# Performance work log

Hardware: AMD Instinct MI355X
Metric: run time of the kernel (lower is better)

## Reference

```python
import jax, jax.numpy as jnp
import numpy as np

B, N, L, K = 2, 16384, 256, 4
DIN, DOUT, DLAT, H, A, NH = 2, 3, 64, 128, 32, 4
PI = float(np.pi)

def _lin(key, din, dout, std=None):
    k1, k2 = jax.random.split(key)
    if std is None:
        lim = 1.0 / np.sqrt(din)
        w = jax.random.uniform(k1, (din, dout), minval=-lim, maxval=lim)
        b = jax.random.uniform(k2, (dout,), minval=-lim, maxval=lim)
        return w, b
    return jax.random.normal(k1, (din, dout)) * std

def setup_inputs() -> dict:
    key = jax.random.key(0)
    ks = jax.random.split(key, 16)
    x = jax.random.uniform(ks[0], (B, N, DIN)) * 2.0 - 1.0
    p = jax.random.uniform(ks[1], (B, L, DIN)) * 2.0 - 1.0
    c = jax.random.normal(ks[2], (B, L, DLAT))
    g = jax.random.uniform(ks[3], (B, L, 1)) * 0.5 + 0.1
    W_stem, b_stem = _lin(ks[4], DLAT, H)
    Wq_sin = _lin(ks[5], DIN, H // 2, std=2.0)
    Wq1, bq1 = _lin(ks[6], H + DIN, H)
    Wq2, bq2 = _lin(ks[7], H, NH * A)
    Wv_sin = _lin(ks[8], DIN, H // 2, std=20.0)
    Wv1, bv1 = _lin(ks[9], H + DIN, H)
    Wv2, bv2 = _lin(ks[10], H, 2 * H)
    Wk, bk = _lin(ks[11], H, NH * A)
    Wv, bv = _lin(ks[12], H, NH * H)
    Wo1, bo1 = _lin(ks[13], NH * H, NH * H)
    Wo2, bo2 = _lin(ks[14], NH * H, DOUT)
    return dict(x=x, p=p, c=c, g=g, W_stem=W_stem, b_stem=b_stem,
                Wq_sin=Wq_sin, Wq1=Wq1, bq1=bq1, Wq2=Wq2, bq2=bq2,
                Wv_sin=Wv_sin, Wv1=Wv1, bv1=bv1, Wv2=Wv2, bv2=bv2,
                Wk=Wk, bk=bk, Wv=Wv, bv=bv, Wo1=Wo1, bo1=bo1, Wo2=Wo2, bo2=bo2)

def _sin_emb(coords, W):
    c = PI * (coords + 1.0)
    e = c @ W
    return jnp.sin(jnp.concatenate([c, e, e + PI / 2.0], axis=-1))

def _emb_mlp(coords, Wsin, W1, b1, W2, b2):
    h = _sin_emb(coords, Wsin)
    h = jax.nn.gelu(h @ W1 + b1, approximate=False)
    return h @ W2 + b2

def _gather(t, idx):
    # t: [B,L,D], idx: [B,N,K] -> [B,N,K,D]
    return jax.vmap(lambda tb, ib: tb[ib])(t, idx)

def reference(x, p, c, g, W_stem, b_stem, Wq_sin, Wq1, bq1, Wq2, bq2,
              Wv_sin, Wv1, bv1, Wv2, bv2, Wk, bk, Wv, bv, Wo1, bo1, Wo2, bo2):
    c = c @ W_stem + b_stem                       # [B,L,H]
    k = c @ Wk + bk                               # [B,L,NH*A]
    rel_pos = x[:, :, None, :] - p[:, None, :, :] # [B,N,L,2]
    zx = jnp.sum(rel_pos ** 2, axis=-1)           # [B,N,L]
    idx = jnp.argsort(zx, axis=-1)[:, :, :K]      # [B,N,K]
    zx_k = jnp.take_along_axis(zx, idx, axis=2)[..., None]            # [B,N,K,1]
    rel_k = jnp.take_along_axis(rel_pos, idx[..., None], axis=2)      # [B,N,K,2]
    c_k = _gather(c, idx)                         # [B,N,K,H]
    k_k = _gather(k, idx)                         # [B,N,K,NH*A]
    g_k = _gather(g, idx)                         # [B,N,K,1]
    q = _emb_mlp(rel_k, Wq_sin, Wq1, bq1, Wq2, bq2)                   # [B,N,K,NH*A]
    vgb = _emb_mlp(rel_k, Wv_sin, Wv1, bv1, Wv2, bv2)                 # [B,N,K,2H]
    v_g, v_b = vgb[..., :H], vgb[..., H:]
    v = (c_k * v_g + v_b) @ Wv + bv               # [B,N,K,NH*H]
    q = q.reshape(B, N, K, NH, A)
    k_k = k_k.reshape(B, N, K, NH, A)
    v = v.reshape(B, N, K, NH, H)
    logits = jnp.sum(q * k_k, axis=-1, keepdims=True) \
             - ((1.0 / g_k ** 2) * zx_k)[..., None, :]                # [B,N,K,NH,1]
    att = jax.nn.softmax(logits, axis=2)
    y = jnp.sum(att * v, axis=2).reshape(B, N, NH * H)
    y = jax.nn.gelu(y @ Wo1 + bo1, approximate=False)
    return y @ Wo2 + bo2                          # [B,N,3]
```

## Files before the change

kernel.cpp:

```cpp
#include <hip/hip_runtime.h>
#include <math.h>

typedef unsigned short U16;
typedef unsigned int u32;
typedef unsigned long long u64;
typedef __attribute__((ext_vector_type(8))) short short8;
typedef __attribute__((ext_vector_type(4))) float f4;

#define LPTS   256
#define MFMA16(a,b,c) __builtin_amdgcn_mfma_f32_16x16x32_bf16(a, b, c, 0, 0, 0)

__device__ __forceinline__ float bf2f(U16 u) {
  return __uint_as_float(((unsigned int)u) << 16);
}
__device__ __forceinline__ U16 f2bf(float f) {
  unsigned int x = __float_as_uint(f);
  return (U16)((x + 0x7fffu + ((x >> 16) & 1u)) >> 16);
}
__device__ __forceinline__ u32 pk_bf16(float lo, float hi) {
  u32 r;
  asm("v_cvt_pk_bf16_f32 %0, %1, %2" : "=v"(r) : "v"(lo), "v"(hi));
  return r;
}
__device__ __forceinline__ float gelu_f(float v) {
  float z = fabsf(v) * 0.70710678f;
  float t = __builtin_amdgcn_rcpf(fmaf(0.3275911f, z, 1.0f));
  float poly = t * fmaf(t, fmaf(t, fmaf(t, fmaf(t, 1.061405429f, -1.453152027f),
                                        1.421413741f), -0.284496736f), 0.254829592f);
  float e = __expf(-z * z);
  float erf_abs = fmaf(-poly, e, 1.0f);
  float erf_s = copysignf(erf_abs, v);
  return 0.5f * v * (1.0f + erf_s);
}
__device__ __forceinline__ void ins4(u32& k0, u32& k1, u32& k2, u32& k3, u32 key) {
  if (key < k3) {
    if (key < k0)      { k3 = k2; k2 = k1; k1 = k0; k0 = key; }
    else if (key < k1) { k3 = k2; k2 = k1; k1 = key; }
    else if (key < k2) { k3 = k2; k2 = key; }
    else               { k3 = key; }
  }
}
__device__ __forceinline__ float ldf(const void* s, int i, int mode) {
  return mode ? bf2f(((const U16*)s)[i]) : ((const float*)s)[i];
}
__device__ __forceinline__ int wave_sniff(const void* w4) {
  int lane = threadIdx.x & 63;
  float v = bf2f(((const U16*)w4)[2 * lane]);
  u64 m = __ballot(fabsf(v) <= 0.1251f);
  return (__popcll(m) >= 56) ? 1 : 0;
}

struct PackArgs {
  const void* src[6];
  int K[6], N[6], KS[6];
  int base[7];
};

__global__ __launch_bounds__(256) void enf_prep(PackArgs pa,
    const void* c, const void* Wst, const void* bst, const void* Wkp, const void* bkp,
    float* __restrict__ cp_ws, float* __restrict__ kk_ws, U16* __restrict__ P)
{
  __shared__ float c_s[2][64];
  __shared__ float cp_s[2][128];
  const int t = threadIdx.x;
  const int mode = wave_sniff(Wst);
  const int bid = blockIdx.x;
  if (bid < 204) {
    int u = bid * 256 + t;
    if (u < pa.base[6]) {
      int s = 0;
      while (u >= pa.base[s + 1]) ++s;
      int rel = u - pa.base[s];
      int lane8 = rel & 63, rest = rel >> 6;
      int ks = rest % pa.KS[s], nt = rest / pa.KS[s];
      int kb = ks * 32 + ((lane8 >> 4) * 8);
      int n  = nt * 16 + (lane8 & 15);
      U16 vv[8];
#pragma unroll
      for (int j = 0; j < 8; ++j) {
        int k = kb + j;
        U16 v = 0;
        if (k < pa.K[s]) {
          int off = k * pa.N[s] + n;
          v = mode ? ((const U16*)pa.src[s])[off] : f2bf(((const float*)pa.src[s])[off]);
        }
        vv[j] = v;
      }
      *(short8*)(P + (size_t)u * 8) = *(short8*)vv;
    }
  } else {
    const int half = t >> 7, tl = t & 127;
    const int row = (bid - 204) * 2 + half;
    if (tl < 64) c_s[half][tl] = ldf(c, row * 64 + tl, mode);
    __syncthreads();
    float acc = 0.f;
#pragma unroll 8
    for (int i = 0; i < 64; ++i) acc = fmaf(c_s[half][i], ldf(Wst, i * 128 + tl, mode), acc);
    float cpv = acc + ldf(bst, tl, mode);
    cp_s[half][tl] = cpv;
    cp_ws[row * 128 + tl] = cpv;
    __syncthreads();
    acc = 0.f;
#pragma unroll 8
    for (int i = 0; i < 128; ++i) acc = fmaf(cp_s[half][i], ldf(Wkp, i * 128 + tl, mode), acc);
    kk_ws[row * 128 + tl] = acc + ldf(bkp, tl, mode);
  }
}

__global__ __launch_bounds__(512, 4) void enf_main(
    const void* __restrict__ w4,
    const void* __restrict__ x, const void* __restrict__ p, const void* __restrict__ g,
    const void* __restrict__ Wq_sin, const void* __restrict__ Wv_sin,
    const U16* __restrict__ PWq1, const void* __restrict__ bq1,
    const U16* __restrict__ PWq2, const void* __restrict__ bq2,
    const U16* __restrict__ PWv1, const void* __restrict__ bv1,
    const U16* __restrict__ PWv2, const void* __restrict__ bv2,
    const U16* __restrict__ PWv, const void* __restrict__ bv,
    const U16* __restrict__ PWo1, const void* __restrict__ bo1,
    const void* __restrict__ Wo2, const void* __restrict__ bo2,
    const float* __restrict__ cp_ws, const float* __restrict__ kk_ws,
    void* __restrict__ outp)
{
  __shared__ __align__(16) U16 poolS[128 * 168];
  __shared__ __align__(16) U16 poolH[128 * 132];
  __shared__ float wsin_s[128];
  __shared__ float xq[64];
  __shared__ float selDx[128], selDy[128], selB[128];
  __shared__ float att_s[128 * 4];
  __shared__ U16   selL[128];
  const int t = threadIdx.x;
  const int w = t >> 6, lane = t & 63;
  const int quad = lane >> 4, cl = lane & 15;
  const int qbase = blockIdx.x * 32;
  const int b = qbase >> 14;
  const int mode = wave_sniff(w4);
  float* p_sh = (float*)poolS;

  if (t < 64) xq[t] = ldf(x, qbase * 2 + t, mode);
  if (t < 128) wsin_s[t] = ldf(Wq_sin, t, mode);
  p_sh[t] = ldf(p, b * LPTS * 2 + t, mode);
  __syncthreads();

  {
    const int q = t >> 4;
    const float x0 = xq[q * 2 + 0], x1 = xq[q * 2 + 1];
    const int j = t & 15;
    u32 k0 = ~0u, k1 = ~0u, k2 = ~0u, k3 = ~0u;
#pragma unroll
    for (int s = 0; s < 16; ++s) {
      const int l = j * 16 + s;
      float2 pp = *(const float2*)&p_sh[l * 2];
      float dx = __fsub_rn(x0, pp.x);
      float dy = __fsub_rn(x1, pp.y);
      float d  = __fadd_rn(__fmul_rn(dx, dx), __fmul_rn(dy, dy));
      u32 key = (__float_as_uint(d) & 0xFFFFFF00u) | (u32)l;
      ins4(k0, k1, k2, k3, key);
    }
#pragma unroll
    for (int d = 1; d <= 8; d <<= 1) {
      u32 p0 = __shfl_xor(k0, d, 16);
      u32 p1 = __shfl_xor(k1, d, 16);
      u32 p2 = __shfl_xor(k2, d, 16);
      u32 p3 = __shfl_xor(k3, d, 16);
      ins4(k0, k1, k2, k3, p0); ins4(k0, k1, k2, k3, p1);
      ins4(k0, k1, k2, k3, p2); ins4(k0, k1, k2, k3, p3);
    }
    if (j == 0) {
      u32 sel[4] = { k0, k1, k2, k3 };
#pragma unroll
      for (int k = 0; k < 4; ++k) {
        int l = (int)(sel[k] & 255u);
        int r = q * 4 + k;
        selL[r]  = (U16)l;
        float dx = __fsub_rn(x0, p_sh[l * 2 + 0]);
        float dy = __fsub_rn(x1, p_sh[l * 2 + 1]);
        float zx = __fadd_rn(__fmul_rn(dx, dx), __fmul_rn(dy, dy));
        selDx[r] = dx;
        selDy[r] = dy;
        float gf = ldf(g, b * LPTS + l, mode);
        selB[r]  = __fmul_rn(1.0f / __fmul_rn(gf, gf), zx);
      }
    }
  }
  __syncthreads();

  {
    const int r = t >> 2, ln = t & 3;
    const float dx = selDx[r], dy = selDy[r];
    const float c0 = 3.14159274f * (dx + 1.0f);
    const float c1 = 3.14159274f * (dy + 1.0f);
    U16* rowp = poolS + r * 168;
    if (ln == 0) rowp[0] = f2bf(__sinf(c0));
    if (ln == 1) rowp[1] = f2bf(__sinf(c1));
#pragma unroll 1
    for (int i = ln * 16; i < ln * 16 + 16; i += 2) {
      float e0 = __fadd_rn(__fmul_rn(c0, wsin_s[i]),     __fmul_rn(c1, wsin_s[64 + i]));
      float e1 = __fadd_rn(__fmul_rn(c0, wsin_s[i + 1]), __fmul_rn(c1, wsin_s[64 + i + 1]));
      *(u32*)(rowp + 2 + i)  = pk_bf16(__sinf(e0), __sinf(e1));
      *(u32*)(rowp + 66 + i) = pk_bf16(__sinf(e0 + 1.57079637f), __sinf(e1 + 1.57079637f));
    }
#pragma unroll 1
    for (int k = ln; k < 15; k += 4) *(u32*)(rowp + 130 + 2 * k) = 0;
  }
  float wv_tmp = (t < 128) ? ldf(Wv_sin, t, mode) : 0.f;
  short8 h4b0 = *(const short8*)(PWq1 + ((w * 5) * 64 + lane) * 8);
  __syncthreads();

  if (t < 128) wsin_s[t] = wv_tmp;
  {
    f4 acc[8];
#pragma unroll
    for (int i = 0; i < 8; ++i) acc[i] = (f4){0.f, 0.f, 0.f, 0.f};
    const U16* pb0 = PWq1 + ((w * 5) * 64 + lane) * 8;
    short8 b0 = h4b0;
#pragma unroll 1
    for (int ks = 0; ks < 5; ++ks) {
      short8 n0 = *(const short8*)(pb0 + (ks + 1) * 512);
#pragma unroll
      for (int mt = 0; mt < 8; ++mt) {
        short8 a = *(const short8*)(poolS + (mt * 16 + cl) * 168 + quad * 8 + ks * 32);
        acc[mt] = MFMA16(a, b0, acc[mt]);
      }
      b0 = n0;
    }
    int col = w * 16 + cl;
    float bb = ldf(bq1, col, mode);
#pragma unroll
    for (int mt = 0; mt < 8; ++mt)
#pragma unroll
      for (int reg = 0; reg < 4; ++reg)
        poolH[(mt * 16 + quad * 4 + reg) * 132 + col] = f2bf(gelu_f(acc[mt][reg] + bb));
  }
  short8 h5b0 = *(const short8*)(PWq2 + ((2 * (w & 3) + 0) * 4 * 64 + lane) * 8);
  short8 h5b1 = *(const short8*)(PWq2 + ((2 * (w & 3) + 1) * 4 * 64 + lane) * 8);
  __syncthreads();

  if (w < 4) {
    const int wl = w;
    f4 acc[2][8];
#pragma unroll
    for (int i = 0; i < 8; ++i) { acc[0][i] = (f4){0.f,0.f,0.f,0.f}; acc[1][i] = (f4){0.f,0.f,0.f,0.f}; }
    const U16* pb0 = PWq2 + ((2 * wl + 0) * 4 * 64 + lane) * 8;
    const U16* pb1 = PWq2 + ((2 * wl + 1) * 4 * 64 + lane) * 8;
    short8 b0 = h5b0;
    short8 b1 = h5b1;
#pragma unroll 1
    for (int ks = 0; ks < 4; ++ks) {
      short8 n0 = *(const short8*)(pb0 + (ks + 1) * 512);
      short8 n1 = *(const short8*)(pb1 + (ks + 1) * 512);
#pragma unroll
      for (int mt = 0; mt < 8; ++mt) {
        short8 a = *(const short8*)(poolH + (mt * 16 + cl) * 132 + quad * 8 + ks * 32);
        acc[0][mt] = MFMA16(a, b0, acc[0][mt]);
        acc[1][mt] = MFMA16(a, b1, acc[1][mt]);
      }
      b0 = n0; b1 = n1;
    }
    const float bq2c0 = ldf(bq2, (2 * wl + 0) * 16 + cl, mode);
    const float bq2c1 = ldf(bq2, (2 * wl + 1) * 16 + cl, mode);
    const float* kkb = kk_ws + (size_t)b * LPTS * 128;
#pragma unroll
    for (int mt = 0; mt < 8; ++mt) {
      float part[4];
#pragma unroll
      for (int reg = 0; reg < 4; ++reg) {
        int r = mt * 16 + quad * 4 + reg;
        const float* kr = kkb + selL[r] * 128;
        float q0 = acc[0][mt][reg] + bq2c0;
        float q1 = acc[1][mt][reg] + bq2c1;
        part[reg] = __fmul_rn(q0, kr[(2 * wl + 0) * 16 + cl]);
        part[reg] = fmaf(q1, kr[(2 * wl + 1) * 16 + cl], part[reg]);
      }
#pragma unroll
      for (int d = 1; d <= 8; d <<= 1) {
        part[0] += __shfl_xor(part[0], d, 16);
        part[1] += __shfl_xor(part[1], d, 16);
        part[2] += __shfl_xor(part[2], d, 16);
        part[3] += __shfl_xor(part[3], d, 16);
      }
      {
        int q = mt * 4 + quad;
        float pr = (cl & 2) ? ((cl & 1) ? part[3] : part[2])
                            : ((cl & 1) ? part[1] : part[0]);
        float lg = pr - selB[q * 4 + (cl & 3)];
        float m = fmaxf(lg, __shfl_xor(lg, 1, 4));
        m = fmaxf(m, __shfl_xor(m, 2, 4));
        float e = __expf(lg - m);
        float s = e + __shfl_xor(e, 1, 4);
        s = s + __shfl_xor(s, 2, 4);
        if (cl < 4) att_s[(q * 4 + cl) * 4 + wl] = e / s;
      }
    }
  } else {
    const int tt = t - 256;
    const int r = tt >> 1, ln2 = tt & 1;
    const float dx = selDx[r], dy = selDy[r];
    const float c0 = 3.14159274f * (dx + 1.0f);
    const float c1 = 3.14159274f * (dy + 1.0f);
    U16* rowp = poolS + r * 168;
    if (ln2 == 0) rowp[0] = f2bf(__sinf(c0));
    if (ln2 == 1) rowp[1] = f2bf(__sinf(c1));
#pragma unroll 1
    for (int i = ln2 * 32; i < ln2 * 32 + 32; i += 2) {
      float e0 = __fadd_rn(__fmul_rn(c0, wsin_s[i]),     __fmul_rn(c1, wsin_s[64 + i]));
      float e1 = __fadd_rn(__fmul_rn(c0, wsin_s[i + 1]), __fmul_rn(c1, wsin_s[64 + i + 1]));
      *(u32*)(rowp + 2 + i)  = pk_bf16(__sinf(e0), __sinf(e1));
      *(u32*)(rowp + 66 + i) = pk_bf16(__sinf(e0 + 1.57079637f), __sinf(e1 + 1.57079637f));
    }
#pragma unroll 1
    for (int k = ln2; k < 15; k += 2) *(u32*)(rowp + 130 + 2 * k) = 0;
  }
  short8 h6b0 = *(const short8*)(PWv1 + ((w * 5) * 64 + lane) * 8);
  __syncthreads();

  {
    f4 acc[8];
#pragma unroll
    for (int i = 0; i < 8; ++i) acc[i] = (f4){0.f, 0.f, 0.f, 0.f};
    const U16* pb0 = PWv1 + ((w * 5) * 64 + lane) * 8;
    short8 b0 = h6b0;
#pragma unroll 1
    for (int ks = 0; ks < 5; ++ks) {
      short8 n0 = *(const short8*)(pb0 + (ks + 1) * 512);
#pragma unroll
      for (int mt = 0; mt < 8; ++mt) {
        short8 a = *(const short8*)(poolS + (mt * 16 + cl) * 168 + quad * 8 + ks * 32);
        acc[mt] = MFMA16(a, b0, acc[mt]);
      }
      b0 = n0;
    }
    int col = w * 16 + cl;
    float bb = ldf(bv1, col, mode);
#pragma unroll
    for (int mt = 0; mt < 8; ++mt)
#pragma unroll
      for (int reg = 0; reg < 4; ++reg)
        poolH[(mt * 16 + quad * 4 + reg) * 132 + col] = f2bf(gelu_f(acc[mt][reg] + bb));
  }
  short8 h7g = *(const short8*)(PWv2 + ((w * 4) * 64 + lane) * 8);
  short8 h7b = *(const short8*)(PWv2 + (((8 + w) * 4) * 64 + lane) * 8);
  __syncthreads();

  {
    f4 ag[8], ab[8];
#pragma unroll
    for (int i = 0; i < 8; ++i) { ag[i] = (f4){0.f,0.f,0.f,0.f}; ab[i] = (f4){0.f,0.f,0.f,0.f}; }
    const U16* pg = PWv2 + ((w * 4) * 64 + lane) * 8;
    const U16* pb = PWv2 + (((8 + w) * 4) * 64 + lane) * 8;
    short8 bg = h7g;
    short8 bb2 = h7b;
#pragma unroll 1
    for (int ks = 0; ks < 4; ++ks) {
      short8 ng = *(const short8*)(pg + (ks + 1) * 512);
      short8 nb = *(const short8*)(pb + (ks + 1) * 512);
#pragma unroll
      for (int mt = 0; mt < 8; ++mt) {
        short8 a = *(const short8*)(poolH + (mt * 16 + cl) * 132 + quad * 8 + ks * 32);
        ag[mt] = MFMA16(a, bg, ag[mt]);
        ab[mt] = MFMA16(a, bb2, ab[mt]);
      }
      bg = ng; bb2 = nb;
    }
    int col = w * 16 + cl;
    float bgb = ldf(bv2, col, mode), bbb = ldf(bv2, 128 + col, mode);
#pragma unroll
    for (int mt = 0; mt < 8; ++mt)
#pragma unroll
      for (int reg = 0; reg < 4; ++reg) {
        int row = mt * 16 + quad * 4 + reg;
        float cp = cp_ws[(b * LPTS + selL[row]) * 128 + col];
        float vin = __fadd_rn(__fmul_rn(cp, ag[mt][reg] + bgb), ab[mt][reg] + bbb);
        poolS[row * 132 + col] = f2bf(vin);
      }
  }
  short8 h9cb0 = *(const short8*)(PWv + (((w >> 1) * 8 + (w & 1) * 4 + 0) * 4 * 64 + lane) * 8);
  short8 h9cb1 = *(const short8*)(PWv + (((w >> 1) * 8 + (w & 1) * 4 + 1) * 4 * 64 + lane) * 8);
  short8 h9cb2 = *(const short8*)(PWv + (((w >> 1) * 8 + (w & 1) * 4 + 2) * 4 * 64 + lane) * 8);
  short8 h9cb3 = *(const short8*)(PWv + (((w >> 1) * 8 + (w & 1) * 4 + 3) * 4 * 64 + lane) * 8);
  __syncthreads();

  {
    const int sl = t & 7;
#pragma unroll 1
    for (int pass = 0; pass < 2; ++pass) {
      int gqh = (t >> 3) + pass * 64;
      int q = gqh & 31, h = gqh >> 5;
      float a0 = att_s[(q * 4 + 0) * 4 + h];
      float a1 = att_s[(q * 4 + 1) * 4 + h];
      float a2 = att_s[(q * 4 + 2) * 4 + h];
      float a3 = att_s[(q * 4 + 3) * 4 + h];
      const U16* v0p = poolS + (q * 4 + 0) * 132;
      const U16* v1p = poolS + (q * 4 + 1) * 132;
      const U16* v2p = poolS + (q * 4 + 2) * 132;
      const U16* v3p = poolS + (q * 4 + 3) * 132;
      U16* up = poolH + (h * 32 + q) * 132;
#pragma unroll 1
      for (int j = 0; j < 8; ++j) {
        int e0 = j * 16 + sl * 2;
        ushort2 v0 = *(const ushort2*)(v0p + e0);
        ushort2 v1 = *(const ushort2*)(v1p + e0);
        ushort2 v2 = *(const ushort2*)(v2p + e0);
        ushort2 v3 = *(const ushort2*)(v3p + e0);
        float s0 = fmaf(a3, bf2f(v3.x), fmaf(a2, bf2f(v2.x), fmaf(a1, bf2f(v1.x), a0 * bf2f(v0.x))));
        float s1 = fmaf(a3, bf2f(v3.y), fmaf(a2, bf2f(v2.y), fmaf(a1, bf2f(v1.y), a0 * bf2f(v0.y))));
        *(u32*)(up + e0) = pk_bf16(s0, s1);
      }
    }
  }
  __syncthreads();

  U16* ySt = poolS;
  {
    f4 acc5[2][4];
#pragma unroll
    for (int i = 0; i < 4; ++i) { acc5[0][i] = (f4){0.f,0.f,0.f,0.f}; acc5[1][i] = (f4){0.f,0.f,0.f,0.f}; }
    const int h = w >> 1;
    const int nt0 = h * 8 + (w & 1) * 4;
    const U16* a5p = poolH + (h * 32 + cl) * 132 + quad * 8;
    short8 cb[4], nb[4];
    cb[0] = h9cb0; cb[1] = h9cb1; cb[2] = h9cb2; cb[3] = h9cb3;
#pragma unroll 1
    for (int ks = 0; ks < 4; ++ks) {
#pragma unroll
      for (int ntl = 0; ntl < 4; ++ntl)
        nb[ntl] = *(const short8*)(PWv + (((nt0 + ntl) * 4 + ks + 1) * 64 + lane) * 8);
#pragma unroll
      for (int mt = 0; mt < 2; ++mt) {
        short8 a = *(const short8*)(a5p + mt * 16 * 132 + ks * 32);
#pragma unroll
        for (int ntl = 0; ntl < 4; ++ntl) acc5[mt][ntl] = MFMA16(a, cb[ntl], acc5[mt][ntl]);
      }
#pragma unroll
      for (int ntl = 0; ntl < 4; ++ntl) cb[ntl] = nb[ntl];
    }
#pragma unroll
    for (int ntl = 0; ntl < 4; ++ntl) {
      int col = (nt0 + ntl) * 16 + cl;
      float bbv = ldf(bv, col, mode);
#pragma unroll
      for (int mt = 0; mt < 2; ++mt)
#pragma unroll
        for (int reg = 0; reg < 4; ++reg) {
          int q = mt * 16 + quad * 4 + reg;
          ySt[q * 520 + col] = f2bf(acc5[mt][ntl][reg] + bbv);
        }
    }
  }
  short8 hAcb0 = *(const short8*)(PWo1 + (((w * 4 + 0) * 16) * 64 + lane) * 8);
  short8 hAcb1 = *(const short8*)(PWo1 + (((w * 4 + 1) * 16) * 64 + lane) * 8);
  short8 hAcb2 = *(const short8*)(PWo1 + (((w * 4 + 2) * 16) * 64 + lane) * 8);
  short8 hAcb3 = *(const short8*)(PWo1 + (((w * 4 + 3) * 16) * 64 + lane) * 8);
  __syncthreads();

  {
    f4 acc[2][4];
#pragma unroll
    for (int i = 0; i < 4; ++i) { acc[0][i] = (f4){0.f,0.f,0.f,0.f}; acc[1][i] = (f4){0.f,0.f,0.f,0.f}; }
    const U16* aP = ySt + cl * 520 + quad * 8;
    const U16* bP = PWo1 + ((w * 4) * 16 * 64 + lane) * 8;
    short8 cb[4], nb[4];
    cb[0] = hAcb0; cb[1] = hAcb1; cb[2] = hAcb2; cb[3] = hAcb3;
#pragma unroll 1
    for (int ks = 0; ks < 16; ++ks) {
#pragma unroll
      for (int ntl = 0; ntl < 4; ++ntl)
        nb[ntl] = *(const short8*)(bP + (ntl * 16 + ks + 1) * 512);
#pragma unroll
      for (int mt = 0; mt < 2; ++mt) {
        short8 a = *(const short8*)(aP + mt * 16 * 520 + ks * 32);
#pragma unroll
        for (int ntl = 0; ntl < 4; ++ntl) acc[mt][ntl] = MFMA16(a, cb[ntl], acc[mt][ntl]);
      }
#pragma unroll
      for (int ntl = 0; ntl < 4; ++ntl) cb[ntl] = nb[ntl];
    }
    float oacc[2][4][3];
#pragma unroll
    for (int mt = 0; mt < 2; ++mt)
#pragma unroll
      for (int reg = 0; reg < 4; ++reg) { oacc[mt][reg][0]=0.f; oacc[mt][reg][1]=0.f; oacc[mt][reg][2]=0.f; }
#pragma unroll
    for (int ntl = 0; ntl < 4; ++ntl) {
      int col = (w * 4 + ntl) * 16 + cl;
      float bb = ldf(bo1, col, mode);
      float w0 = ldf(Wo2, col * 3 + 0, mode);
      float w1 = ldf(Wo2, col * 3 + 1, mode);
      float w2 = ldf(Wo2, col * 3 + 2, mode);
#pragma unroll
      for (int mt = 0; mt < 2; ++mt)
#pragma unroll
        for (int reg = 0; reg < 4; ++reg) {
          float y2 = gelu_f(acc[mt][ntl][reg] + bb);
          oacc[mt][reg][0] = fmaf(y2, w0, oacc[mt][reg][0]);
          oacc[mt][reg][1] = fmaf(y2, w1, oacc[mt][reg][1]);
          oacc[mt][reg][2] = fmaf(y2, w2, oacc[mt][reg][2]);
        }
    }
    float* obuf = (float*)poolH;
#pragma unroll
    for (int mt = 0; mt < 2; ++mt)
#pragma unroll
      for (int reg = 0; reg < 4; ++reg)
#pragma unroll
        for (int cix = 0; cix < 3; ++cix) {
          float v = oacc[mt][reg][cix];
          v += __shfl_xor(v, 1);
          v += __shfl_xor(v, 2);
          v += __shfl_xor(v, 4);
          v += __shfl_xor(v, 8);
          if (cl == 0) obuf[(w * 32 + mt * 16 + quad * 4 + reg) * 3 + cix] = v;
        }
  }
  __syncthreads();
  if (t < 96) {
    float* obuf = (float*)poolH;
    int row = t / 3, cix = t - row * 3;
    float s = obuf[row * 3 + cix];
#pragma unroll
    for (int ww = 1; ww < 8; ++ww) s += obuf[(ww * 32 + row) * 3 + cix];
    float ov = s + ldf(bo2, cix, mode);
    int pos = (qbase + row) * 3 + cix;
    if (mode) ((U16*)outp)[pos] = f2bf(ov);
    else      ((float*)outp)[pos] = ov;
  }
}

extern "C" void kernel_launch(void* const* d_in, const int* in_sizes, int n_in,
                              void* d_out, int out_size, void* d_ws, size_t ws_size,
                              hipStream_t stream) {
  (void)in_sizes; (void)n_in; (void)out_size; (void)ws_size;

  float* ws     = (float*)d_ws;
  float* cp_ws  = ws;
  float* kk_ws  = ws + 65536;
  U16*   Pbase  = (U16*)(ws + 131072);
  U16*   PWq1   = Pbase + 0;
  U16*   PWq2   = Pbase + 20480;
  U16*   PWv1   = Pbase + 36864;
  U16*   PWv2   = Pbase + 57344;
  U16*   PWv    = Pbase + 90112;
  U16*   PWo1   = Pbase + 155648;

  PackArgs pa;
  const int psrc[6] = {7, 9, 12, 14, 18, 20};
  static const int pK[6]  = {130, 128, 130, 128, 128, 512};
  static const int pN[6]  = {128, 128, 128, 256, 512, 512};
  static const int pKS[6] = {5, 4, 5, 4, 4, 16};
  static const int pB8[7] = {0, 2560, 4608, 7168, 11264, 19456, 52224};
  for (int i = 0; i < 6; ++i) {
    pa.src[i] = d_in[psrc[i]];
    pa.K[i] = pK[i]; pa.N[i] = pN[i]; pa.KS[i] = pKS[i]; pa.base[i] = pB8[i];
  }
  pa.base[6] = pB8[6];

  hipLaunchKernelGGL(enf_prep, dim3(460), dim3(256), 0, stream,
                     pa, d_in[2], d_in[4], d_in[5], d_in[16], d_in[17],
                     cp_ws, kk_ws, Pbase);
  hipLaunchKernelGGL(enf_main, dim3(1024), dim3(512), 0, stream,
                     d_in[4],
                     d_in[0], d_in[1], d_in[3],
                     d_in[6], d_in[11],
                     PWq1, d_in[8],  PWq2, d_in[10],
                     PWv1, d_in[13], PWv2, d_in[15],
                     PWv,  d_in[19],
                     PWo1, d_in[21], d_in[22], d_in[23],
                     cp_ws, kk_ws, (void*)d_out);
}
```

Before: 266.8 us.

## Double queries per block to 64 with 1024-thread blocks

Result: slower. 286.6 us (+7.4%).

```diff
diff --git a/kernel.cpp b/kernel.cpp
--- a/kernel.cpp
+++ b/kernel.cpp
@@ -107,7 +107,7 @@
   }
 }
 
-__global__ __launch_bounds__(512, 4) void enf_main(
+__global__ __launch_bounds__(1024, 4) void enf_main(
     const void* __restrict__ w4,
     const void* __restrict__ x, const void* __restrict__ p, const void* __restrict__ g,
     const void* __restrict__ Wq_sin, const void* __restrict__ Wv_sin,
@@ -121,24 +121,26 @@
     const float* __restrict__ cp_ws, const float* __restrict__ kk_ws,
     void* __restrict__ outp)
 {
-  __shared__ __align__(16) U16 poolS[128 * 168];
-  __shared__ __align__(16) U16 poolH[128 * 132];
+  __shared__ __align__(16) U16 poolS[256 * 168];
+  __shared__ __align__(16) U16 poolH[256 * 132];
   __shared__ float wsin_s[128];
-  __shared__ float xq[64];
-  __shared__ float selDx[128], selDy[128], selB[128];
-  __shared__ float att_s[128 * 4];
-  __shared__ U16   selL[128];
+  __shared__ float xq[128];
+  __shared__ float selDx[256], selDy[256], selB[256];
+  __shared__ float att_s[256 * 4];
+  __shared__ U16   selL[256];
   const int t = threadIdx.x;
   const int w = t >> 6, lane = t & 63;
   const int quad = lane >> 4, cl = lane & 15;
-  const int qbase = blockIdx.x * 32;
+  const int wt = w >> 1;
+  const int rH = (w & 1) * 128;
+  const int qbase = blockIdx.x * 64;
   const int b = qbase >> 14;
   const int mode = wave_sniff(w4);
   float* p_sh = (float*)poolS;
 
-  if (t < 64) xq[t] = ldf(x, qbase * 2 + t, mode);
-  if (t < 128) wsin_s[t] = ldf(Wq_sin, t, mode);
-  p_sh[t] = ldf(p, b * LPTS * 2 + t, mode);
+  if (t < 512) p_sh[t] = ldf(p, b * LPTS * 2 + t, mode);
+  else if (t < 640) xq[t - 512] = ldf(x, qbase * 2 + (t - 512), mode);
+  else if (t < 768) wsin_s[t - 640] = ldf(Wq_sin, t - 640, mode);
   __syncthreads();
 
   {
@@ -203,7 +205,7 @@
     for (int k = ln; k < 15; k += 4) *(u32*)(rowp + 130 + 2 * k) = 0;
   }
   float wv_tmp = (t < 128) ? ldf(Wv_sin, t, mode) : 0.f;
-  short8 h4b0 = *(const short8*)(PWq1 + ((w * 5) * 64 + lane) * 8);
+  short8 h4b0 = *(const short8*)(PWq1 + ((wt * 5) * 64 + lane) * 8);
   __syncthreads();
 
   if (t < 128) wsin_s[t] = wv_tmp;
@@ -211,32 +213,38 @@
     f4 acc[8];
 #pragma unroll
     for (int i = 0; i < 8; ++i) acc[i] = (f4){0.f, 0.f, 0.f, 0.f};
-    const U16* pb0 = PWq1 + ((w * 5) * 64 + lane) * 8;
+    const U16* pb0 = PWq1 + ((wt * 5) * 64 + lane) * 8;
     short8 b0 = h4b0;
 #pragma unroll 1
     for (int ks = 0; ks < 5; ++ks) {
       short8 n0 = *(const short8*)(pb0 + (ks + 1) * 512);
 #pragma unroll
       for (int mt = 0; mt < 8; ++mt) {
-        short8 a = *(const short8*)(poolS + (mt * 16 + cl) * 168 + quad * 8 + ks * 32);
+        short8 a = *(const short8*)(poolS + ((rH + mt * 16 + cl)) * 168 + quad * 8 + ks * 32);
         acc[mt] = MFMA16(a, b0, acc[mt]);
       }
       b0 = n0;
     }
-    int col = w * 16 + cl;
+    int col = wt * 16 + cl;
     float bb = ldf(bq1, col, mode);
 #pragma unroll
     for (int mt = 0; mt < 8; ++mt)
 #pragma unroll
       for (int reg = 0; reg < 4; ++reg)
-        poolH[(mt * 16 + quad * 4 + reg) * 132 + col] = f2bf(gelu_f(acc[mt][reg] + bb));
-  }
-  short8 h5b0 = *(const short8*)(PWq2 + ((2 * (w & 3) + 0) * 4 * 64 + lane) * 8);
-  short8 h5b1 = *(const short8*)(PWq2 + ((2 * (w & 3) + 1) * 4 * 64 + lane) * 8);
-  __syncthreads();
-
-  if (w < 4) {
-    const int wl = w;
+        poolH[(rH + mt * 16 + quad * 4 + reg) * 132 + col] = f2bf(gelu_f(acc[mt][reg] + bb));
+  }
+  {
+  }
+  short8 h5b0, h5b1;
+  {
+    int hw = wt & 3;
+    h5b0 = *(const short8*)(PWq2 + ((2 * hw + 0) * 4 * 64 + lane) * 8);
+    h5b1 = *(const short8*)(PWq2 + ((2 * hw + 1) * 4 * 64 + lane) * 8);
+  }
+  __syncthreads();
+
+  if (w < 8) {
+    const int wl = wt;
     f4 acc[2][8];
 #pragma unroll
     for (int i = 0; i < 8; ++i) { acc[0][i] = (f4){0.f,0.f,0.f,0.f}; acc[1][i] = (f4){0.f,0.f,0.f,0.f}; }
@@ -250,7 +258,7 @@
       short8 n1 = *(const short8*)(pb1 + (ks + 1) * 512);
 #pragma unroll
       for (int mt = 0; mt < 8; ++mt) {
-        short8 a = *(const short8*)(poolH + (mt * 16 + cl) * 132 + quad * 8 + ks * 32);
+        short8 a = *(const short8*)(poolH + (rH + mt * 16 + cl) * 132 + quad * 8 + ks * 32);
         acc[0][mt] = MFMA16(a, b0, acc[0][mt]);
         acc[1][mt] = MFMA16(a, b1, acc[1][mt]);
       }
@@ -264,7 +272,7 @@
       float part[4];
 #pragma unroll
       for (int reg = 0; reg < 4; ++reg) {
-        int r = mt * 16 + quad * 4 + reg;
+        int r = rH + mt * 16 + quad * 4 + reg;
         const float* kr = kkb + selL[r] * 128;
         float q0 = acc[0][mt][reg] + bq2c0;
         float q1 = acc[1][mt][reg] + bq2c1;
@@ -279,7 +287,7 @@
         part[3] += __shfl_xor(part[3], d, 16);
       }
       {
-        int q = mt * 4 + quad;
+        int q = (rH >> 2) + mt * 4 + quad;
         float pr = (cl & 2) ? ((cl & 1) ? part[3] : part[2])
                             : ((cl & 1) ? part[1] : part[0]);
         float lg = pr - selB[q * 4 + (cl & 3)];
@@ -292,7 +300,7 @@
       }
     }
   } else {
-    const int tt = t - 256;
+    const int tt = t - 512;
     const int r = tt >> 1, ln2 = tt & 1;
     const float dx = selDx[r], dy = selDy[r];
     const float c0 = 3.14159274f * (dx + 1.0f);
@@ -310,43 +318,43 @@
 #pragma unroll 1
     for (int k = ln2; k < 15; k += 2) *(u32*)(rowp + 130 + 2 * k) = 0;
   }
-  short8 h6b0 = *(const short8*)(PWv1 + ((w * 5) * 64 + lane) * 8);
+  short8 h6b0 = *(const short8*)(PWv1 + ((wt * 5) * 64 + lane) * 8);
   __syncthreads();
 
   {
     f4 acc[8];
 #pragma unroll
     for (int i = 0; i < 8; ++i) acc[i] = (f4){0.f, 0.f, 0.f, 0.f};
-    const U16* pb0 = PWv1 + ((w * 5) * 64 + lane) * 8;
+    const U16* pb0 = PWv1 + ((wt * 5) * 64 + lane) * 8;
     short8 b0 = h6b0;
 #pragma unroll 1
     for (int ks = 0; ks < 5; ++ks) {
       short8 n0 = *(const short8*)(pb0 + (ks + 1) * 512);
 #pragma unroll
       for (int mt = 0; mt < 8; ++mt) {
-        short8 a = *(const short8*)(poolS + (mt * 16 + cl) * 168 + quad * 8 + ks * 32);
+        short8 a = *(const short8*)(poolS + (rH + mt * 16 + cl) * 168 + quad * 8 + ks * 32);
         acc[mt] = MFMA16(a, b0, acc[mt]);
       }
       b0 = n0;
     }
-    int col = w * 16 + cl;
+    int col = wt * 16 + cl;
     float bb = ldf(bv1, col, mode);
 #pragma unroll
     for (int mt = 0; mt < 8; ++mt)
 #pragma unroll
       for (int reg = 0; reg < 4; ++reg)
-        poolH[(mt * 16 + quad * 4 + reg) * 132 + col] = f2bf(gelu_f(acc[mt][reg] + bb));
-  }
-  short8 h7g = *(const short8*)(PWv2 + ((w * 4) * 64 + lane) * 8);
-  short8 h7b = *(const short8*)(PWv2 + (((8 + w) * 4) * 64 + lane) * 8);
+        poolH[(rH + mt * 16 + quad * 4 + reg) * 132 + col] = f2bf(gelu_f(acc[mt][reg] + bb));
+  }
+  short8 h7g = *(const short8*)(PWv2 + ((wt * 4) * 64 + lane) * 8);
+  short8 h7b = *(const short8*)(PWv2 + (((8 + wt) * 4) * 64 + lane) * 8);
   __syncthreads();
 
   {
     f4 ag[8], ab[8];
 #pragma unroll
     for (int i = 0; i < 8; ++i) { ag[i] = (f4){0.f,0.f,0.f,0.f}; ab[i] = (f4){0.f,0.f,0.f,0.f}; }
-    const U16* pg = PWv2 + ((w * 4) * 64 + lane) * 8;
-    const U16* pb = PWv2 + (((8 + w) * 4) * 64 + lane) * 8;
+    const U16* pg = PWv2 + ((wt * 4) * 64 + lane) * 8;
+    const U16* pb = PWv2 + (((8 + wt) * 4) * 64 + lane) * 8;
     short8 bg = h7g;
     short8 bb2 = h7b;
 #pragma unroll 1
@@ -355,36 +363,37 @@
       short8 nb = *(const short8*)(pb + (ks + 1) * 512);
 #pragma unroll
       for (int mt = 0; mt < 8; ++mt) {
-        short8 a = *(const short8*)(poolH + (mt * 16 + cl) * 132 + quad * 8 + ks * 32);
+        short8 a = *(const short8*)(poolH + (rH + mt * 16 + cl) * 132 + quad * 8 + ks * 32);
         ag[mt] = MFMA16(a, bg, ag[mt]);
         ab[mt] = MFMA16(a, bb2, ab[mt]);
       }
       bg = ng; bb2 = nb;
     }
-    int col = w * 16 + cl;
+    int col = wt * 16 + cl;
     float bgb = ldf(bv2, col, mode), bbb = ldf(bv2, 128 + col, mode);
 #pragma unroll
     for (int mt = 0; mt < 8; ++mt)
 #pragma unroll
       for (int reg = 0; reg < 4; ++reg) {
-        int row = mt * 16 + quad * 4 + reg;
+        int row = rH + mt * 16 + quad * 4 + reg;
         float cp = cp_ws[(b * LPTS + selL[row]) * 128 + col];
         float vin = __fadd_rn(__fmul_rn(cp, ag[mt][reg] + bgb), ab[mt][reg] + bbb);
         poolS[row * 132 + col] = f2bf(vin);
       }
   }
-  short8 h9cb0 = *(const short8*)(PWv + (((w >> 1) * 8 + (w & 1) * 4 + 0) * 4 * 64 + lane) * 8);
-  short8 h9cb1 = *(const short8*)(PWv + (((w >> 1) * 8 + (w & 1) * 4 + 1) * 4 * 64 + lane) * 8);
-  short8 h9cb2 = *(const short8*)(PWv + (((w >> 1) * 8 + (w & 1) * 4 + 2) * 4 * 64 + lane) * 8);
-  short8 h9cb3 = *(const short8*)(PWv + (((w >> 1) * 8 + (w & 1) * 4 + 3) * 4 * 64 + lane) * 8);
+  const int p9h = w >> 2, p9rH = ((w >> 1) & 1) * 32, p9nt0 = (w >> 2) * 8 + (w & 1) * 4;
+  short8 h9cb0 = *(const short8*)(PWv + ((p9nt0 + 0) * 4 * 64 + lane) * 8);
+  short8 h9cb1 = *(const short8*)(PWv + ((p9nt0 + 1) * 4 * 64 + lane) * 8);
+  short8 h9cb2 = *(const short8*)(PWv + ((p9nt0 + 2) * 4 * 64 + lane) * 8);
+  short8 h9cb3 = *(const short8*)(PWv + ((p9nt0 + 3) * 4 * 64 + lane) * 8);
   __syncthreads();
 
   {
     const int sl = t & 7;
 #pragma unroll 1
     for (int pass = 0; pass < 2; ++pass) {
-      int gqh = (t >> 3) + pass * 64;
-      int q = gqh & 31, h = gqh >> 5;
+      int gqh = (t >> 3) + pass * 128;
+      int q = gqh & 63, h = gqh >> 6;
       float a0 = att_s[(q * 4 + 0) * 4 + h];
       float a1 = att_s[(q * 4 + 1) * 4 + h];
       float a2 = att_s[(q * 4 + 2) * 4 + h];
@@ -393,7 +402,7 @@
       const U16* v1p = poolS + (q * 4 + 1) * 132;
       const U16* v2p = poolS + (q * 4 + 2) * 132;
       const U16* v3p = poolS + (q * 4 + 3) * 132;
-      U16* up = poolH + (h * 32 + q) * 132;
+      U16* up = poolH + (h * 64 + q) * 132;
 #pragma unroll 1
       for (int j = 0; j < 8; ++j) {
         int e0 = j * 16 + sl * 2;
@@ -414,16 +423,14 @@
     f4 acc5[2][4];
 #pragma unroll
     for (int i = 0; i < 4; ++i) { acc5[0][i] = (f4){0.f,0.f,0.f,0.f}; acc5[1][i] = (f4){0.f,0.f,0.f,0.f}; }
-    const int h = w >> 1;
-    const int nt0 = h * 8 + (w & 1) * 4;
-    const U16* a5p = poolH + (h * 32 + cl) * 132 + quad * 8;
+    const U16* a5p = poolH + (p9h * 64 + p9rH + cl) * 132 + quad * 8;
     short8 cb[4], nb[4];
     cb[0] = h9cb0; cb[1] = h9cb1; cb[2] = h9cb2; cb[3] = h9cb3;
 #pragma unroll 1
     for (int ks = 0; ks < 4; ++ks) {
 #pragma unroll
       for (int ntl = 0; ntl < 4; ++ntl)
-        nb[ntl] = *(const short8*)(PWv + (((nt0 + ntl) * 4 + ks + 1) * 64 + lane) * 8);
+        nb[ntl] = *(const short8*)(PWv + (((p9nt0 + ntl) * 4 + ks + 1) * 64 + lane) * 8);
 #pragma unroll
       for (int mt = 0; mt < 2; ++mt) {
         short8 a = *(const short8*)(a5p + mt * 16 * 132 + ks * 32);
@@ -435,59 +442,57 @@
     }
 #pragma unroll
     for (int ntl = 0; ntl < 4; ++ntl) {
-      int col = (nt0 + ntl) * 16 + cl;
+      int col = (p9nt0 + ntl) * 16 + cl;
       float bbv = ldf(bv, col, mode);
 #pragma unroll
       for (int mt = 0; mt < 2; ++mt)
 #pragma unroll
         for (int reg = 0; reg < 4; ++reg) {
-          int q = mt * 16 + quad * 4 + reg;
+          int q = p9rH + mt * 16 + quad * 4 + reg;
           ySt[q * 520 + col] = f2bf(acc5[mt][ntl][reg] + bbv);
         }
     }
   }
-  short8 hAcb0 = *(const short8*)(PWo1 + (((w * 4 + 0) * 16) * 64 + lane) * 8);
-  short8 hAcb1 = *(const short8*)(PWo1 + (((w * 4 + 1) * 16) * 64 + lane) * 8);
-  short8 hAcb2 = *(const short8*)(PWo1 + (((w * 4 + 2) * 16) * 64 + lane) * 8);
-  short8 hAcb3 = *(const short8*)(PWo1 + (((w * 4 + 3) * 16) * 64 + lane) * 8);
-  __syncthreads();
-
-  {
-    f4 acc[2][4];
-#pragma unroll
-    for (int i = 0; i < 4; ++i) { acc[0][i] = (f4){0.f,0.f,0.f,0.f}; acc[1][i] = (f4){0.f,0.f,0.f,0.f}; }
+  short8 hAcb0 = *(const short8*)(PWo1 + (((w * 2 + 0) * 16) * 64 + lane) * 8);
+  short8 hAcb1 = *(const short8*)(PWo1 + (((w * 2 + 1) * 16) * 64 + lane) * 8);
+  __syncthreads();
+
+  {
+    f4 acc[4][2];
+#pragma unroll
+    for (int i = 0; i < 4; ++i) { acc[i][0] = (f4){0.f,0.f,0.f,0.f}; acc[i][1] = (f4){0.f,0.f,0.f,0.f}; }
     const U16* aP = ySt + cl * 520 + quad * 8;
-    const U16* bP = PWo1 + ((w * 4) * 16 * 64 + lane) * 8;
-    short8 cb[4], nb[4];
-    cb[0] = hAcb0; cb[1] = hAcb1; cb[2] = hAcb2; cb[3] = hAcb3;
+    const U16* bP = PWo1 + ((w * 2) * 16 * 64 + lane) * 8;
+    short8 cb[2], nb[2];
+    cb[0] = hAcb0; cb[1] = hAcb1;
 #pragma unroll 1
     for (int ks = 0; ks < 16; ++ks) {
 #pragma unroll
-      for (int ntl = 0; ntl < 4; ++ntl)
+      for (int ntl = 0; ntl < 2; ++ntl)
         nb[ntl] = *(const short8*)(bP + (ntl * 16 + ks + 1) * 512);
 #pragma unroll
-      for (int mt = 0; mt < 2; ++mt) {
+      for (int mt = 0; mt < 4; ++mt) {
         short8 a = *(const short8*)(aP + mt * 16 * 520 + ks * 32);
 #pragma unroll
-        for (int ntl = 0; ntl < 4; ++ntl) acc[mt][ntl] = MFMA16(a, cb[ntl], acc[mt][ntl]);
-      }
-#pragma unroll
-      for (int ntl = 0; ntl < 4; ++ntl) cb[ntl] = nb[ntl];
-    }
-    float oacc[2][4][3];
-#pragma unroll
-    for (int mt = 0; mt < 2; ++mt)
+        for (int ntl = 0; ntl < 2; ++ntl) acc[mt][ntl] = MFMA16(a, cb[ntl], acc[mt][ntl]);
+      }
+#pragma unroll
+      for (int ntl = 0; ntl < 2; ++ntl) cb[ntl] = nb[ntl];
+    }
+    float oacc[4][4][3];
+#pragma unroll
+    for (int mt = 0; mt < 4; ++mt)
 #pragma unroll
       for (int reg = 0; reg < 4; ++reg) { oacc[mt][reg][0]=0.f; oacc[mt][reg][1]=0.f; oacc[mt][reg][2]=0.f; }
 #pragma unroll
-    for (int ntl = 0; ntl < 4; ++ntl) {
-      int col = (w * 4 + ntl) * 16 + cl;
+    for (int ntl = 0; ntl < 2; ++ntl) {
+      int col = (w * 2 + ntl) * 16 + cl;
       float bb = ldf(bo1, col, mode);
       float w0 = ldf(Wo2, col * 3 + 0, mode);
       float w1 = ldf(Wo2, col * 3 + 1, mode);
       float w2 = ldf(Wo2, col * 3 + 2, mode);
 #pragma unroll
-      for (int mt = 0; mt < 2; ++mt)
+      for (int mt = 0; mt < 4; ++mt)
 #pragma unroll
         for (int reg = 0; reg < 4; ++reg) {
           float y2 = gelu_f(acc[mt][ntl][reg] + bb);
@@ -498,7 +503,7 @@
     }
     float* obuf = (float*)poolH;
 #pragma unroll
-    for (int mt = 0; mt < 2; ++mt)
+    for (int mt = 0; mt < 4; ++mt)
 #pragma unroll
       for (int reg = 0; reg < 4; ++reg)
 #pragma unroll
@@ -508,16 +513,16 @@
           v += __shfl_xor(v, 2);
           v += __shfl_xor(v, 4);
           v += __shfl_xor(v, 8);
-          if (cl == 0) obuf[(w * 32 + mt * 16 + quad * 4 + reg) * 3 + cix] = v;
+          if (cl == 0) obuf[(w * 64 + mt * 16 + quad * 4 + reg) * 3 + cix] = v;
         }
   }
   __syncthreads();
-  if (t < 96) {
+  if (t < 192) {
     float* obuf = (float*)poolH;
     int row = t / 3, cix = t - row * 3;
     float s = obuf[row * 3 + cix];
 #pragma unroll
-    for (int ww = 1; ww < 8; ++ww) s += obuf[(ww * 32 + row) * 3 + cix];
+    for (int ww = 1; ww < 16; ++ww) s += obuf[(ww * 64 + row) * 3 + cix];
     float ov = s + ldf(bo2, cix, mode);
     int pos = (qbase + row) * 3 + cix;
     if (mode) ((U16*)outp)[pos] = f2bf(ov);
@@ -556,7 +561,7 @@
   hipLaunchKernelGGL(enf_prep, dim3(460), dim3(256), 0, stream,
                      pa, d_in[2], d_in[4], d_in[5], d_in[16], d_in[17],
                      cp_ws, kk_ws, Pbase);
-  hipLaunchKernelGGL(enf_main, dim3(1024), dim3(512), 0, stream,
+  hipLaunchKernelGGL(enf_main, dim3(512), dim3(1024), 0, stream,
                      d_in[4],
                      d_in[0], d_in[1], d_in[3],
                      d_in[6], d_in[11],
```
